# Kernel optimization log

Measured on AMD Instinct MI355X. Metric: run time of the kernel, lower is better.

Reference implementation:

```python
import jax, jax.numpy as jnp
import numpy as np

E = 100000      # number of edges
MUL = 64        # multiplicity of each irrep (0e and 1o)
DIM = MUL * 1 + MUL * 3  # 256 feature dim for 64x0e + 64x1o

INV_SQRT3 = 1.0 / np.sqrt(3.0)          # wigner-3j value for (0,1,1) and (1,1,0) paths
ALPHA0 = 1.0 / np.sqrt(2.0 * MUL * MUL)  # path norm: 2 paths feed the 0e output
ALPHA1 = 1.0 / np.sqrt(2.0 * MUL * MUL)  # path norm: 2 paths feed the 1o output


def _split(t):
    # t: [E, 256] -> scalars [E, MUL], vectors [E, MUL, 3]
    s = t[:, :MUL]
    v = t[:, MUL:].reshape(-1, MUL, 3)
    return s, v


def fc_tensor_product(x, y, W000, W110, W011, W101):
    """FullyConnectedTensorProduct(64x0e+64x1o, 64x0e+64x1o -> 64x0e+64x1o).

    Paths (uvw-connected, one weight [MUL,MUL,MUL] each):
      (0e,0e)->0e : cg = 1
      (1o,1o)->0e : cg = delta_ij / sqrt(3)
      (0e,1o)->1o : cg = delta_jk / sqrt(3)
      (1o,0e)->1o : cg = delta_ik / sqrt(3)
    """
    x0, x1 = _split(x)
    y0, y1 = _split(y)
    out0 = ALPHA0 * (
        jnp.einsum('eu,ev,uvw->ew', x0, y0, W000)
        + INV_SQRT3 * jnp.einsum('eui,evi,uvw->ew', x1, y1, W110)
    )
    out1 = ALPHA1 * INV_SQRT3 * (
        jnp.einsum('eu,evi,uvw->ewi', x0, y1, W011)
        + jnp.einsum('eui,ev,uvw->ewi', x1, y0, W101)
    )
    return jnp.concatenate([out0, out1.reshape(-1, MUL * 3)], axis=1)


def setup_inputs() -> dict:
    key = jax.random.key(0)
    ks = jax.random.split(key, 12)
    mk = lambda k, shape: jax.random.normal(k, shape, dtype=jnp.float32)
    return {
        'e1x': mk(ks[0], (E, DIM)),
        'e1y': mk(ks[1], (E, DIM)),
        'e2x': mk(ks[2], (E, DIM)),
        'e2y': mk(ks[3], (E, DIM)),
        'W1_000': mk(ks[4], (MUL, MUL, MUL)),
        'W1_110': mk(ks[5], (MUL, MUL, MUL)),
        'W1_011': mk(ks[6], (MUL, MUL, MUL)),
        'W1_101': mk(ks[7], (MUL, MUL, MUL)),
        'W2_000': mk(ks[8], (MUL, MUL, MUL)),
        'W2_110': mk(ks[9], (MUL, MUL, MUL)),
        'W2_011': mk(ks[10], (MUL, MUL, MUL)),
        'W2_101': mk(ks[11], (MUL, MUL, MUL)),
    }


def reference(e1x, e1y, e2x, e2y,
              W1_000, W1_110, W1_011, W1_101,
              W2_000, W2_110, W2_011, W2_101) -> jnp.ndarray:
    # SimpleEdgeBlock.forward: sum of one fully-connected TP per input tuple
    out = fc_tensor_product(e1x, e1y, W1_000, W1_110, W1_011, W1_101)
    out = out + fc_tensor_product(e2x, e2y, W2_000, W2_110, W2_011, W2_101)
    return out
```

## Files before the change

### kernel.cpp

```cpp
#include <hip/hip_runtime.h>
#include <stdint.h>


typedef __attribute__((ext_vector_type(8))) short short8;
typedef __attribute__((ext_vector_type(16))) float f32x16;
typedef unsigned short u16;

#define ETOT 100000

__device__ __forceinline__ unsigned pk2(float lo, float hi) {
  return __builtin_amdgcn_perm(__builtin_bit_cast(unsigned, hi),
                               __builtin_bit_cast(unsigned, lo), 0x07060302u);
}
__device__ __forceinline__ void unpk8(short8 s, float f[8]) {
  uint4 u = __builtin_bit_cast(uint4, s);
  unsigned a[4] = {u.x, u.y, u.z, u.w};
#pragma unroll
  for (int jj = 0; jj < 4; ++jj) {
    f[2 * jj]     = __builtin_bit_cast(float, a[jj] << 16);
    f[2 * jj + 1] = __builtin_bit_cast(float, a[jj] & 0xffff0000u);
  }
}
__device__ __forceinline__ short8 scalepack(const float f[8], float ysc) {
  unsigned p0 = pk2(f[0] * ysc, f[1] * ysc);
  unsigned p1 = pk2(f[2] * ysc, f[3] * ysc);
  unsigned p2 = pk2(f[4] * ysc, f[5] * ysc);
  unsigned p3 = pk2(f[6] * ysc, f[7] * ysc);
  uint4 r = make_uint4(p0, p1, p2, p3);
  return __builtin_bit_cast(short8, r);
}
__device__ __forceinline__ short8 pack8(const float f[8]) {
  unsigned p0 = pk2(f[0], f[1]);
  unsigned p1 = pk2(f[2], f[3]);
  unsigned p2 = pk2(f[4], f[5]);
  unsigned p3 = pk2(f[6], f[7]);
  uint4 r = make_uint4(p0, p1, p2, p3);
  return __builtin_bit_cast(short8, r);
}

__device__ __forceinline__ void dma16(const void* g, void* l) {
  __builtin_amdgcn_global_load_lds(
      (const __attribute__((address_space(1))) unsigned*)g,
      (__attribute__((address_space(3))) unsigned*)l, 16, 0, 0);
}
__device__ __forceinline__ void dma4(const void* g, void* l) {
  __builtin_amdgcn_global_load_lds(
      (const __attribute__((address_space(1))) unsigned*)g,
      (__attribute__((address_space(3))) unsigned*)l, 4, 0, 0);
}

__global__ void prep_B(const float* __restrict__ W10, const float* __restrict__ W11,
                       const float* __restrict__ W12, const float* __restrict__ W13,
                       const float* __restrict__ W20, const float* __restrict__ W21,
                       const float* __restrict__ W22, const float* __restrict__ W23,
                       u16* __restrict__ B) {
  int idx = blockIdx.x * 256 + threadIdx.x;
  int j = idx & 7;
  int w = (idx >> 3) & 63;
  int oct = (idx >> 9) & 7;
  int t = (idx >> 12) & 1;
  int s = idx >> 13;
  int klin = s * 64 + oct * 8 + j;
  int p = klin >> 13;
  int r = klin & 8191;
  int v = (r >> 7) & 63;
  int half = (r >> 6) & 1;
  int u = r & 63;
  const float a0 = 0.011048543456039806f;
  const float a0s3 = a0 * 0.5773502691896258f;
  const float* Wsrc;
  float scale;
  if (t == 0) {
    Wsrc = half ? (p ? W21 : W11) : (p ? W20 : W10);
    scale = half ? a0s3 : a0;
  } else {
    Wsrc = half ? (p ? W23 : W13) : (p ? W22 : W12);
    scale = a0s3;
  }
  float val = Wsrc[u * 4096 + v * 64 + w] * scale;
  unsigned ub = __builtin_bit_cast(unsigned, val);
  ub += 0x7fffu + ((ub >> 16) & 1u);
  B[idx] = (u16)(ub >> 16);
}

__global__ __launch_bounds__(128, 2)
void tp_main(const float* __restrict__ e1x, const float* __restrict__ e1y,
             const float* __restrict__ e2x, const float* __restrict__ e2y,
             const u16* __restrict__ B, float* __restrict__ out) {
  __shared__ u16 blds[2][8192];
  __shared__ float yv[2][256];

  const int tid = threadIdx.x;
  const int wv = tid >> 6;
  const int lane = tid & 63;
  const int m = lane & 31;
  const int hw = lane >> 5;
  const int be0 = blockIdx.x * 64;
  const int e0 = be0 + wv * 32;
  const bool active = (e0 < ETOT);
  const int e = e0 + m;

  f32x16 acc[4][2] = {};
  short8 xc[4][4];

  auto issueB = [&](int s1) {
    const int cb = s1 * 1024 + wv * 512;
    const u16* src = B + (size_t)(cb + lane) * 8;
    u16* dst = (u16*)&blds[s1 & 1][(wv * 512) * 8];
#pragma unroll
    for (int q = 0; q < 8; ++q) dma16(src + q * 64 * 8, dst + q * 64 * 8);
  };
  auto issueY = [&](int g) {
    const int b2 = g & 1;
    if (g > 127) g = 127;
    const float* Ysrc = (g >> 6) ? e2y : e1y;
    const int v = g & 63;
#pragma unroll
    for (int q = 0; q < 2; ++q) {
      int f = wv * 128 + q * 64 + lane;
      int el = f >> 2, ch = f & 3;
      int eg = be0 + el;
      if (eg > ETOT - 1) eg = ETOT - 1;
      const float* src = Ysrc + (size_t)eg * 256 + (ch == 0 ? v : 64 + v * 3 + (ch - 1));
      dma4(src, &yv[b2][wv * 128 + q * 64]);
    }
  };

  issueY(0);
  issueB(0);

#pragma unroll 1
  for (int p = 0; p < 2; ++p) {
    const float* X = p ? e2x : e1x;

    if (active) {
#pragma unroll
      for (int q = 0; q < 4; ++q) {
        const float* px = X + (size_t)e * 256 + q * 16 + hw * 8;
        float4 a4 = *(const float4*)px;
        float4 b4 = *(const float4*)(px + 4);
        float f[8] = {a4.x, a4.y, a4.z, a4.w, b4.x, b4.y, b4.z, b4.w};
        xc[0][q] = pack8(f);
      }
#pragma unroll
      for (int i = 0; i < 3; ++i) {
        const float* px = X + (size_t)e * 256 + 64 + i;
#pragma unroll
        for (int q = 0; q < 4; ++q) {
          float f[8];
#pragma unroll
          for (int j = 0; j < 8; ++j) f[j] = px[(q * 16 + hw * 8 + j) * 3];
          xc[1 + i][q] = pack8(f);
        }
      }
    }

#pragma unroll 1
    for (int sl = 0; sl < 128; ++sl) {
      const int s = p * 128 + sl;
      issueB(s + 1 > 255 ? 255 : s + 1);
      if (!(s & 1)) issueY((s >> 1) + 1);
      asm volatile("s_waitcnt vmcnt(10)" ::: "memory");
      __builtin_amdgcn_sched_barrier(0);
      __builtin_amdgcn_s_barrier();

      const int h = s & 1;
      const int g = s >> 1;
      const u16* bb = blds[s & 1];
      if (active) {
        float4 ysv = *(const float4*)&yv[g & 1][(wv * 32 + m) * 4];
#pragma unroll
        for (int uq = 0; uq < 4; ++uq) {
          short8 bfrag[2][2];
#pragma unroll
          for (int tb = 0; tb < 2; ++tb)
#pragma unroll
            for (int n = 0; n < 2; ++n)
              bfrag[tb][n] =
                  *(const short8*)&bb[(tb * 512 + (uq * 2 + hw) * 64 + n * 32 + m) * 8];
          short8 af[4];
          if (h == 0) {
            float xf[8];
            unpk8(xc[0][uq], xf);
            af[0] = scalepack(xf, ysv.x);
            af[1] = scalepack(xf, ysv.y);
            af[2] = scalepack(xf, ysv.z);
            af[3] = scalepack(xf, ysv.w);
          } else {
            float x0f[8], x1f[8], x2f[8];
            unpk8(xc[1][uq], x0f);
            unpk8(xc[2][uq], x1f);
            unpk8(xc[3][uq], x2f);
            float z[8];
#pragma unroll
            for (int j = 0; j < 8; ++j)
              z[j] = x0f[j] * ysv.y + x1f[j] * ysv.z + x2f[j] * ysv.w;
            af[0] = pack8(z);
            af[1] = scalepack(x0f, ysv.x);
            af[2] = scalepack(x1f, ysv.x);
            af[3] = scalepack(x2f, ysv.x);
          }
          __builtin_amdgcn_s_setprio(1);
#pragma unroll
          for (int t = 0; t < 4; ++t) {
            const int tb = t ? 1 : 0;
            acc[t][0] = __builtin_amdgcn_mfma_f32_32x32x16_bf16(
                af[t], bfrag[tb][0], acc[t][0], 0, 0, 0);
            acc[t][1] = __builtin_amdgcn_mfma_f32_32x32x16_bf16(
                af[t], bfrag[tb][1], acc[t][1], 0, 0, 0);
          }
          __builtin_amdgcn_s_setprio(0);
        }
      }
      asm volatile("s_waitcnt lgkmcnt(0)" ::: "memory");
      __builtin_amdgcn_sched_barrier(0);
      __builtin_amdgcn_s_barrier();
    }
  }

  if (active) {
#pragma unroll
    for (int t = 0; t < 4; ++t)
#pragma unroll
      for (int n0 = 0; n0 < 2; ++n0) {
        f32x16 c = acc[t][n0];
        int n = n0 * 32 + m;
#pragma unroll
        for (int r = 0; r < 16; ++r) {
          int row = (r & 3) + 8 * (r >> 2) + 4 * hw;
          int ee = e0 + row;
          size_t off;
          if (t == 0) off = (size_t)ee * 256 + n;
          else        off = (size_t)ee * 256 + 64 + n * 3 + (t - 1);
          out[off] = c[r];
        }
      }
  }
}

extern "C" void kernel_launch(void* const* d_in, const int* in_sizes, int n_in,
                              void* d_out, int out_size, void* d_ws, size_t ws_size,
                              hipStream_t stream) {
  const float* e1x = (const float*)d_in[0];
  const float* e1y = (const float*)d_in[1];
  const float* e2x = (const float*)d_in[2];
  const float* e2y = (const float*)d_in[3];
  const size_t bElems = (size_t)2 * 64 * 16384;
  if (ws_size < bElems * sizeof(u16)) return;
  u16* B = (u16*)d_ws;
  prep_B<<<8192, 256, 0, stream>>>(
      (const float*)d_in[4], (const float*)d_in[5], (const float*)d_in[6],
      (const float*)d_in[7], (const float*)d_in[8], (const float*)d_in[9],
      (const float*)d_in[10], (const float*)d_in[11], B);
  tp_main<<<(ETOT + 63) / 64, 128, 0, stream>>>(e1x, e1y, e2x, e2y, B,
                                                (float*)d_out);
}
```

Baseline: 2.765 ms.

## Use 4-wave blocks of 128 edges to share each B slice across more waves

The block grows from 2 to 4 waves and covers 128 edges instead of 64. Each staged weight slice in LDS now feeds twice as many edges, so per-block B traffic through L2 is halved. The DMA work for B and Y is split among four waves, Y loads are spread over two steps per group, and the vmcnt wait threshold is adjusted to match. In exchange, barriers now synchronize more waves, there are half as many blocks, and occupancy and LDS limits change.

Result: faster. 2.637 ms (-4.6%).

```diff
diff --git a/kernel.cpp b/kernel.cpp
--- a/kernel.cpp
+++ b/kernel.cpp
@@ -83,19 +83,19 @@
   B[idx] = (u16)(ub >> 16);
 }
 
-__global__ __launch_bounds__(128, 2)
+__global__ __launch_bounds__(256, 2)
 void tp_main(const float* __restrict__ e1x, const float* __restrict__ e1y,
              const float* __restrict__ e2x, const float* __restrict__ e2y,
              const u16* __restrict__ B, float* __restrict__ out) {
   __shared__ u16 blds[2][8192];
-  __shared__ float yv[2][256];
+  __shared__ float yv[2][512];
 
   const int tid = threadIdx.x;
   const int wv = tid >> 6;
   const int lane = tid & 63;
   const int m = lane & 31;
   const int hw = lane >> 5;
-  const int be0 = blockIdx.x * 64;
+  const int be0 = blockIdx.x * 128;
   const int e0 = be0 + wv * 32;
   const bool active = (e0 < ETOT);
   const int e = e0 + m;
@@ -104,29 +104,30 @@
   short8 xc[4][4];
 
   auto issueB = [&](int s1) {
-    const int cb = s1 * 1024 + wv * 512;
-    const u16* src = B + (size_t)(cb + lane) * 8;
-    u16* dst = (u16*)&blds[s1 & 1][(wv * 512) * 8];
-#pragma unroll
-    for (int q = 0; q < 8; ++q) dma16(src + q * 64 * 8, dst + q * 64 * 8);
+    const int b = s1 & 1;
+    const u16* src =
+        B + (size_t)s1 * 8192 + (size_t)(wv * 4) * 512 + (size_t)lane * 8;
+#pragma unroll
+    for (int q = 0; q < 4; ++q)
+      dma16(src + q * 512, &blds[b][(wv * 4 + q) * 512]);
   };
-  auto issueY = [&](int g) {
-    const int b2 = g & 1;
+  auto issueYhalf = [&](int g, int h) {
+    const int bg = g & 1;
     if (g > 127) g = 127;
     const float* Ysrc = (g >> 6) ? e2y : e1y;
     const int v = g & 63;
-#pragma unroll
-    for (int q = 0; q < 2; ++q) {
-      int f = wv * 128 + q * 64 + lane;
-      int el = f >> 2, ch = f & 3;
-      int eg = be0 + el;
-      if (eg > ETOT - 1) eg = ETOT - 1;
-      const float* src = Ysrc + (size_t)eg * 256 + (ch == 0 ? v : 64 + v * 3 + (ch - 1));
-      dma4(src, &yv[b2][wv * 128 + q * 64]);
-    }
+    const int i = h * 4 + wv;
+    const int f = i * 64 + lane;
+    const int el = f >> 2, ch = f & 3;
+    int eg = be0 + el;
+    if (eg > ETOT - 1) eg = ETOT - 1;
+    const float* src =
+        Ysrc + (size_t)eg * 256 + (ch == 0 ? v : 64 + v * 3 + (ch - 1));
+    dma4(src, &yv[bg][i * 64]);
   };
 
-  issueY(0);
+  issueYhalf(0, 0);
+  issueYhalf(0, 1);
   issueB(0);
 
 #pragma unroll 1
@@ -159,8 +160,8 @@
     for (int sl = 0; sl < 128; ++sl) {
       const int s = p * 128 + sl;
       issueB(s + 1 > 255 ? 255 : s + 1);
-      if (!(s & 1)) issueY((s >> 1) + 1);
-      asm volatile("s_waitcnt vmcnt(10)" ::: "memory");
+      issueYhalf((s >> 1) + 1, s & 1);
+      asm volatile("s_waitcnt vmcnt(5)" ::: "memory");
       __builtin_amdgcn_sched_barrier(0);
       __builtin_amdgcn_s_barrier();
 
@@ -252,6 +253,6 @@
       (const float*)d_in[4], (const float*)d_in[5], (const float*)d_in[6],
       (const float*)d_in[7], (const float*)d_in[8], (const float*)d_in[9],
       (const float*)d_in[10], (const float*)d_in[11], B);
-  tp_main<<<(ETOT + 63) / 64, 128, 0, stream>>>(e1x, e1y, e2x, e2y, B,
-                                                (float*)d_out);
-}
+  tp_main<<<(ETOT + 127) / 128, 256, 0, stream>>>(e1x, e1y, e2x, e2y, B,
+                                                  (float*)d_out);
+}
```
